# Kernel tuning notes

Hardware: AMD Instinct MI355X
Metric: run time of the kernel (lower is better)

## Reference

```python
import jax, jax.numpy as jnp
import numpy as np

N_NODES = 50000
N_EDGES = 800000
D_IN = 128
D_H = 128
N_LAYERS = 3
N_CLASSES = 10
NUM_GRAPHS = 256
BN_EPS = 1e-5


def _bn(h, gamma, beta):
    # BatchNorm1d, training-mode statistics (biased variance) over node axis
    mu = jnp.mean(h, axis=0)
    var = jnp.mean((h - mu) ** 2, axis=0)
    return (h - mu) * jax.lax.rsqrt(var + BN_EPS) * gamma + beta


def setup_inputs() -> dict:
    key = jax.random.key(0)
    ks = jax.random.split(key, 16)
    x = jax.random.normal(ks[0], (N_NODES, D_IN), dtype=jnp.float32)
    edge_index = jax.random.randint(ks[1], (2, N_EDGES), 0, N_NODES, dtype=jnp.int64)
    batch = jnp.sort(jax.random.randint(ks[2], (N_NODES,), 0, NUM_GRAPHS, dtype=jnp.int64))
    s1 = 1.0 / np.sqrt(D_IN)
    s2 = 1.0 / np.sqrt(D_H)
    W1 = jax.random.uniform(ks[3], (N_LAYERS, D_IN, D_H), jnp.float32, -s1, s1)
    b1 = jax.random.uniform(ks[4], (N_LAYERS, D_H), jnp.float32, -s1, s1)
    g1 = jnp.ones((N_LAYERS, D_H), jnp.float32)
    bt1 = jnp.zeros((N_LAYERS, D_H), jnp.float32)
    W2 = jax.random.uniform(ks[5], (N_LAYERS, D_H, D_H), jnp.float32, -s2, s2)
    b2 = jax.random.uniform(ks[6], (N_LAYERS, D_H), jnp.float32, -s2, s2)
    g2 = jnp.ones((N_LAYERS, D_H), jnp.float32)
    bt2 = jnp.zeros((N_LAYERS, D_H), jnp.float32)
    sc = 1.0 / np.sqrt(D_H * N_LAYERS)
    Wc1 = jax.random.uniform(ks[7], (D_H * N_LAYERS, D_H), jnp.float32, -sc, sc)
    bc1 = jax.random.uniform(ks[8], (D_H,), jnp.float32, -sc, sc)
    Wc2 = jax.random.uniform(ks[9], (D_H, N_CLASSES), jnp.float32, -s2, s2)
    bc2 = jax.random.uniform(ks[10], (N_CLASSES,), jnp.float32, -s2, s2)
    return {"x": x, "edge_index": edge_index, "batch": batch,
            "W1": W1, "b1": b1, "g1": g1, "bt1": bt1,
            "W2": W2, "b2": b2, "g2": g2, "bt2": bt2,
            "Wc1": Wc1, "bc1": bc1, "Wc2": Wc2, "bc2": bc2}


def reference(x, edge_index, batch, W1, b1, g1, bt1, W2, b2, g2, bt2, Wc1, bc1, Wc2, bc2):
    src = edge_index[0]
    dst = edge_index[1]
    readouts = []
    h = x
    for i in range(N_LAYERS):
        # GINConv, eps=0: (1+eps)*h + sum_{j->i} h_j, then MLP
        agg = jax.ops.segment_sum(h[src], dst, num_segments=N_NODES)  # [N, d]
        z = h + agg
        z = z @ W1[i] + b1[i]
        z = jax.nn.relu(_bn(z, g1[i], bt1[i]))
        z = z @ W2[i] + b2[i]
        # outer BN + ReLU
        h = jax.nn.relu(_bn(z, g2[i], bt2[i]))
        readouts.append(jax.ops.segment_sum(h, batch, num_segments=NUM_GRAPHS))
    h_graph = jnp.concatenate(readouts, axis=1)  # [G, L*d]
    # classifier (dropout in eval mode -> identity)
    out = jax.nn.relu(h_graph @ Wc1 + bc1) @ Wc2 + bc2
    return out
```

## Files before the change

### kernel.cpp

```cpp
#include <hip/hip_runtime.h>

#define N_NODES 50000
#define N_EDGES 800000
#define D 128
#define NLAYERS 3
#define N_CLASSES 10
#define NUM_GRAPHS 256
#define BN_EPS 1e-5f

#define CHUNKS 64
#define CHSIZE 12500
#define RANGES 4
#define RSIZE 12500
#define SBANKS 8

typedef __attribute__((ext_vector_type(4))) float f4;
typedef __attribute__((ext_vector_type(2))) float f2;
typedef __attribute__((ext_vector_type(8))) short short8;
typedef __attribute__((ext_vector_type(4))) unsigned short us4;
typedef __attribute__((ext_vector_type(8))) unsigned short us8;

__device__ inline float b2f(unsigned short u) {
    unsigned int i = ((unsigned int)u) << 16;
    return __builtin_bit_cast(float, i);
}
__device__ inline unsigned short f2b(float f) {
    unsigned int u = __builtin_bit_cast(unsigned int, f);
    unsigned int r = (u + 0x7FFFu + ((u >> 16) & 1u)) >> 16;
    return (unsigned short)r;
}

__device__ inline void coef_to_lds(const float* __restrict__ stats,
                                   const float* __restrict__ g,
                                   const float* __restrict__ bt,
                                   float* ac_sm, int tid) {
    if (tid < D) {
        float s = 0.f, q = 0.f;
#pragma unroll
        for (int b = 0; b < SBANKS; b++) {
            s += stats[b * 2 * D + tid];
            q += stats[b * 2 * D + D + tid];
        }
        float mu = s * (1.0f / N_NODES);
        float var = q * (1.0f / N_NODES) - mu * mu;
        float inv = rsqrtf(var + BN_EPS);
        float a = g[tid] * inv;
        ac_sm[tid] = a;
        ac_sm[D + tid] = bt[tid] - mu * a;
    }
}


__global__ __launch_bounds__(256) void k_ph(const int* __restrict__ dst,
                                            int* __restrict__ pos,
                                            int* __restrict__ ph) {
    __shared__ int h[RSIZE];
    int c = blockIdx.x, r = blockIdx.y;
    int t = threadIdx.x;
    for (int i = t; i < RSIZE; i += 256) h[i] = 0;
    __syncthreads();
    int base = c * CHSIZE;
    int lo = r * RSIZE;
    for (int j = t; j < CHSIZE; j += 256) {
        int d = dst[base + j] - lo;
        if ((unsigned)d < RSIZE) pos[base + j] = atomicAdd(&h[d], 1);
    }
    __syncthreads();
    int* outp = ph + (size_t)c * N_NODES + lo;
    for (int i = t; i < RSIZE; i += 256) outp[i] = h[i];
}

__global__ __launch_bounds__(256) void k_merge(int* __restrict__ ph, int* __restrict__ deg) {
    int b = blockIdx.x * 256 + threadIdx.x;
    if (b >= N_NODES) return;
    int s = 0;
#pragma unroll 4
    for (int c = 0; c < CHUNKS; c++) {
        int v = ph[(size_t)c * N_NODES + b];
        ph[(size_t)c * N_NODES + b] = s;
        s += v;
    }
    deg[b] = s;
}


__global__ __launch_bounds__(256) void k_xw(const float* __restrict__ x,
                                            const float* __restrict__ W1,
                                            const float* __restrict__ W2,
                                            us4* __restrict__ xb,
                                            short8* __restrict__ Wb) {
    int gid = blockIdx.x * 256 + threadIdx.x;
    const f4* xf = (const f4*)x;
#pragma unroll
    for (int rep = 0; rep < 2; rep++) {
        int i = gid + rep * 800000;
        f4 v = xf[i];
        us4 o;
        o[0] = f2b(v.x); o[1] = f2b(v.y); o[2] = f2b(v.z); o[3] = f2b(v.w);
        xb[i] = o;
    }
    if (gid < 6 * 32 * 64) {
        int m = gid >> 11;
        int f = (gid >> 6) & 31;
        int l = gid & 63;
        int ct = f >> 2, ks = f & 3;
        int n = ct * 16 + (l & 15);
        int k0 = ks * 32 + (l >> 4) * 8;
        const float* Wsrc = (m < 3) ? (W1 + (size_t)m * D * D) : (W2 + (size_t)(m - 3) * D * D);
        short8 o;
#pragma unroll
        for (int j = 0; j < 8; j++) o[j] = (short)f2b(Wsrc[(size_t)(k0 + j) * D + n]);
        Wb[gid] = o;
    }
}


__global__ void k_s1(const int* __restrict__ deg, const int* __restrict__ bat,
                     int* __restrict__ bsum, int* __restrict__ gp) {
    __shared__ int sm[256];
    int t = threadIdx.x;
    int i = blockIdx.x * 256 + t;
    int v = (i < N_NODES) ? deg[i] : 0;
    sm[t] = v;
    __syncthreads();
    for (int off = 128; off > 0; off >>= 1) {
        if (t < off) sm[t] += sm[t + off];
        __syncthreads();
    }
    if (t == 0) bsum[blockIdx.x] = sm[0];
    if (i < N_NODES) {
        int b = bat[i];
        int prev = (i == 0) ? -1 : bat[i - 1];
        for (int g = prev + 1; g <= b; g++) gp[g] = i;
        if (i == N_NODES - 1)
            for (int g = b + 1; g <= NUM_GRAPHS; g++) gp[g] = N_NODES;
    }
}

__global__ void k_s2(int* __restrict__ bsum, int* __restrict__ rowp) {
    __shared__ int sm[256];
    int t = threadIdx.x;
    int v = (t < 196) ? bsum[t] : 0;
    sm[t] = v;
    __syncthreads();
    for (int off = 1; off < 256; off <<= 1) {
        int u = (t >= off) ? sm[t - off] : 0;
        __syncthreads();
        sm[t] += u;
        __syncthreads();
    }
    if (t < 196) bsum[t] = sm[t] - v;
    if (t == 195) rowp[N_NODES] = sm[t];
}

__global__ void k_s3(const int* __restrict__ deg, const int* __restrict__ bsum,
                     int* __restrict__ rowp) {
    __shared__ int sm[256];
    int t = threadIdx.x;
    int i = blockIdx.x * 256 + t;
    int v = (i < N_NODES) ? deg[i] : 0;
    sm[t] = v;
    __syncthreads();
    for (int off = 1; off < 256; off <<= 1) {
        int u = (t >= off) ? sm[t - off] : 0;
        __syncthreads();
        sm[t] += u;
        __syncthreads();
    }
    if (i < N_NODES) rowp[i] = bsum[blockIdx.x] + sm[t] - v;
}

__global__ __launch_bounds__(256) void k_scatter(const int* __restrict__ src,
                                                 const int* __restrict__ dst,
                                                 const int* __restrict__ pos,
                                                 const int* __restrict__ ph,
                                                 const int* __restrict__ rowp,
                                                 int* __restrict__ csr) {
    int e = blockIdx.x * 256 + threadIdx.x;
    int c = e / CHSIZE;
    int d = dst[e];
    csr[rowp[d] + ph[(size_t)c * N_NODES + d] + pos[e]] = src[e];
}


template <bool APPLY_T>
__global__ __launch_bounds__(256) void k_agg(const us8* __restrict__ H,
                                             const float* __restrict__ stats,
                                             const float* __restrict__ g,
                                             const float* __restrict__ bt,
                                             const int* __restrict__ rowp,
                                             const int* __restrict__ csr,
                                             us8* __restrict__ U) {
    __shared__ float ac_sm[2 * D];
    int tid = threadIdx.x;
    if (APPLY_T) {
        coef_to_lds(stats, g, bt, ac_sm, tid);
        __syncthreads();
    }
    int gid = blockIdx.x * 256 + tid;
    int node = gid >> 4;
    int lane = tid & 15;
    float av[8], cv[8];
    if (APPLY_T) {
#pragma unroll
        for (int i = 0; i < 8; i++) {
            av[i] = ac_sm[lane * 8 + i];
            cv[i] = ac_sm[D + lane * 8 + i];
        }
    }
    float s[8] = {0.f, 0.f, 0.f, 0.f, 0.f, 0.f, 0.f, 0.f};
    auto accum = [&](us8 v) {
#pragma unroll
        for (int i = 0; i < 8; i++) {
            float f = b2f(v[i]);
            if (APPLY_T) f = fmaxf(f * av[i] + cv[i], 0.f);
            s[i] += f;
        }
    };
    accum(H[(size_t)node * 16 + lane]);
    int beg = rowp[node], end = rowp[node + 1];
    int j = beg;
    for (; j + 4 <= end; j += 4) {
        int i0 = csr[j], i1 = csr[j + 1], i2 = csr[j + 2], i3 = csr[j + 3];
        us8 v0 = H[(size_t)i0 * 16 + lane];
        us8 v1 = H[(size_t)i1 * 16 + lane];
        us8 v2 = H[(size_t)i2 * 16 + lane];
        us8 v3 = H[(size_t)i3 * 16 + lane];
        accum(v0); accum(v1); accum(v2); accum(v3);
    }
    for (; j < end; j++) accum(H[(size_t)csr[j] * 16 + lane]);
    us8 o;
#pragma unroll
    for (int i = 0; i < 8; i++) o[i] = f2b(s[i]);
    U[(size_t)node * 16 + lane] = o;
}


template <bool TRANS>
__global__ __launch_bounds__(256) void k_gemm(const unsigned short* __restrict__ A,
                                              const short8* __restrict__ Wb,
                                              const float* __restrict__ bias,
                                              const float* __restrict__ stats_in,
                                              const float* __restrict__ g,
                                              const float* __restrict__ bt,
                                              unsigned short* __restrict__ Z,
                                              float* __restrict__ stats_out, int M) {
    __shared__ float lds_s[D], lds_q[D];
    __shared__ float ac_sm[2 * D];
    int tid = threadIdx.x;
    if (tid < D) { lds_s[tid] = 0.f; lds_q[tid] = 0.f; }
    if (TRANS) coef_to_lds(stats_in, g, bt, ac_sm, tid);
    int w = tid >> 6, l = tid & 63;
    int lr = l & 15, lg = l >> 4;
    int rowb0 = blockIdx.x * 128 + w * 32;
    f4 acc[2][8];
#pragma unroll
    for (int ct = 0; ct < 8; ct++) {
        float bv = bias[ct * 16 + lr];
#pragma unroll
        for (int rt = 0; rt < 2; rt++) {
            acc[rt][ct].x = bv; acc[rt][ct].y = bv; acc[rt][ct].z = bv; acc[rt][ct].w = bv;
        }
    }
    __syncthreads();

#pragma unroll
    for (int ks = 0; ks < 4; ks++) {
        short8 a[2];
#pragma unroll
        for (int rt = 0; rt < 2; rt++) {
            int arow = rowb0 + rt * 16 + lr;
            int arow_c = arow < M ? arow : M - 1;
            if (!TRANS) {
                a[rt] = *(const short8*)(A + (size_t)arow_c * D + ks * 32 + lg * 8);
            } else {
                int k0 = ks * 32 + lg * 8;
                const unsigned short* ap = A + (size_t)arow_c * D + k0;
                us4 v0 = *(const us4*)ap;
                us4 v1 = *(const us4*)(ap + 4);
                f4 a0 = *(const f4*)&ac_sm[k0];
                f4 a1 = *(const f4*)&ac_sm[k0 + 4];
                f4 c0 = *(const f4*)&ac_sm[D + k0];
                f4 c1 = *(const f4*)&ac_sm[D + k0 + 4];
                a[rt][0] = (short)f2b(fmaxf(b2f(v0[0]) * a0.x + c0.x, 0.f));
                a[rt][1] = (short)f2b(fmaxf(b2f(v0[1]) * a0.y + c0.y, 0.f));
                a[rt][2] = (short)f2b(fmaxf(b2f(v0[2]) * a0.z + c0.z, 0.f));
                a[rt][3] = (short)f2b(fmaxf(b2f(v0[3]) * a0.w + c0.w, 0.f));
                a[rt][4] = (short)f2b(fmaxf(b2f(v1[0]) * a1.x + c1.x, 0.f));
                a[rt][5] = (short)f2b(fmaxf(b2f(v1[1]) * a1.y + c1.y, 0.f));
                a[rt][6] = (short)f2b(fmaxf(b2f(v1[2]) * a1.z + c1.z, 0.f));
                a[rt][7] = (short)f2b(fmaxf(b2f(v1[3]) * a1.w + c1.w, 0.f));
            }
        }
#pragma unroll
        for (int ct = 0; ct < 8; ct++) {
            short8 b = Wb[(ct * 4 + ks) * 64 + l];
            acc[0][ct] = __builtin_amdgcn_mfma_f32_16x16x32_bf16(a[0], b, acc[0][ct], 0, 0, 0);
            acc[1][ct] = __builtin_amdgcn_mfma_f32_16x16x32_bf16(a[1], b, acc[1][ct], 0, 0, 0);
        }
    }

#pragma unroll
    for (int ct = 0; ct < 8; ct++) {
        float s = 0.f, q = 0.f;
#pragma unroll
        for (int rt = 0; rt < 2; rt++) {
#pragma unroll
            for (int r = 0; r < 4; r++) {
                float v = acc[rt][ct][r];
                int rd = rowb0 + rt * 16 + lg * 4 + r;
                float m = rd < M ? 1.f : 0.f;
                s += v * m;
                q += v * v * m;
                if (rd < M) Z[(size_t)rd * D + ct * 16 + lr] = f2b(v);
            }
        }
        s += __shfl_xor(s, 16);
        s += __shfl_xor(s, 32);
        q += __shfl_xor(q, 16);
        q += __shfl_xor(q, 32);
        if (lg == 0) {
            atomicAdd(&lds_s[ct * 16 + lr], s);
            atomicAdd(&lds_q[ct * 16 + lr], q);
        }
    }
    __syncthreads();
    int bank = blockIdx.x & (SBANKS - 1);
    if (tid < D) {
        atomicAdd(&stats_out[bank * 2 * D + tid], lds_s[tid]);
        atomicAdd(&stats_out[bank * 2 * D + D + tid], lds_q[tid]);
    }
}


__global__ __launch_bounds__(256) void k_readout(const unsigned int* __restrict__ Zb,
                                                 const float* __restrict__ stats,
                                                 const float* __restrict__ g,
                                                 const float* __restrict__ bt,
                                                 const int* __restrict__ gp,
                                                 const int* __restrict__ batch,
                                                 float* __restrict__ ro, int layer) {
    __shared__ f2 sm[256];
    __shared__ float ac_sm[2 * D];
    int tid = threadIdx.x;
    coef_to_lds(stats, g, bt, ac_sm, tid);
    __syncthreads();
    int n0 = blockIdx.x * 256;
    int n1 = n0 + 256; if (n1 > N_NODES) n1 = N_NODES;
    int g_lo = batch[n0], g_hi = batch[n1 - 1];
    int grp = tid >> 6, cw = tid & 63;
    float a0 = ac_sm[2 * cw], a1 = ac_sm[2 * cw + 1];
    float c0 = ac_sm[D + 2 * cw], c1 = ac_sm[D + 2 * cw + 1];
    for (int gg = g_lo; gg <= g_hi; gg++) {
        int beg = gp[gg]; if (beg < n0) beg = n0;
        int end = gp[gg + 1]; if (end > n1) end = n1;
        f2 acc; acc.x = 0.f; acc.y = 0.f;
        for (int r = beg + grp; r < end; r += 4) {
            unsigned int v = Zb[(size_t)r * 64 + cw];
            float x0 = b2f((unsigned short)(v & 0xFFFFu));
            float x1 = b2f((unsigned short)(v >> 16));
            acc.x += fmaxf(x0 * a0 + c0, 0.f);
            acc.y += fmaxf(x1 * a1 + c1, 0.f);
        }
        sm[tid] = acc;
        __syncthreads();
        if (tid < 64) {
            f2 t = sm[tid];
            t.x += sm[tid + 64].x + sm[tid + 128].x + sm[tid + 192].x;
            t.y += sm[tid + 64].y + sm[tid + 128].y + sm[tid + 192].y;
            atomicAdd(&ro[(size_t)gg * (NLAYERS * D) + layer * D + 2 * cw], t.x);
            atomicAdd(&ro[(size_t)gg * (NLAYERS * D) + layer * D + 2 * cw + 1], t.y);
        }
        __syncthreads();
    }
}


__global__ void k_cls(const float* __restrict__ ro, const float* __restrict__ Wc1,
                      const float* __restrict__ bc1, const float* __restrict__ Wc2,
                      const float* __restrict__ bc2, float* __restrict__ out) {
    __shared__ float r_sm[NLAYERS * D];
    __shared__ float h_sm[D];
    int g = blockIdx.x;
    int t = threadIdx.x;
    for (int i = t; i < NLAYERS * D; i += D) r_sm[i] = ro[(size_t)g * (NLAYERS * D) + i];
    __syncthreads();
    float acc = bc1[t];
    for (int k = 0; k < NLAYERS * D; k++) acc += r_sm[k] * Wc1[(size_t)k * D + t];
    h_sm[t] = fmaxf(acc, 0.f);
    __syncthreads();
    if (t < N_CLASSES) {
        float o = bc2[t];
        for (int k = 0; k < D; k++) o += h_sm[k] * Wc2[k * N_CLASSES + t];
        out[g * N_CLASSES + t] = o;
    }
}


extern "C" void kernel_launch(void* const* d_in, const int* in_sizes, int n_in,
                              void* d_out, int out_size, void* d_ws, size_t ws_size,
                              hipStream_t stream) {
    const float* x   = (const float*)d_in[0];
    const int*   ei  = (const int*)d_in[1];
    const int*   bat = (const int*)d_in[2];
    const float* W1  = (const float*)d_in[3];
    const float* b1  = (const float*)d_in[4];
    const float* g1  = (const float*)d_in[5];
    const float* bt1 = (const float*)d_in[6];
    const float* W2  = (const float*)d_in[7];
    const float* b2  = (const float*)d_in[8];
    const float* g2  = (const float*)d_in[9];
    const float* bt2 = (const float*)d_in[10];
    const float* Wc1 = (const float*)d_in[11];
    const float* bc1 = (const float*)d_in[12];
    const float* Wc2 = (const float*)d_in[13];
    const float* bc2 = (const float*)d_in[14];
    float* out = (float*)d_out;

    const int* src = ei;
    const int* dst = ei + N_EDGES;

    char* ws = (char*)d_ws;
    size_t off = 0;
    auto alloc = [&](size_t bytes) -> void* {
        void* p = ws + off;
        off += (bytes + 255) & ~(size_t)255;
        return p;
    };
    float* stats = (float*)alloc(6 * SBANKS * 2 * D * sizeof(float));
    float* ro    = (float*)alloc((size_t)NUM_GRAPHS * NLAYERS * D * sizeof(float));
    size_t zero_bytes = off;
    int*   deg   = (int*)alloc(N_NODES * sizeof(int));
    int*   gp    = (int*)alloc((NUM_GRAPHS + 1) * sizeof(int));
    int*   bsum  = (int*)alloc(256 * sizeof(int));
    int*   rowp  = (int*)alloc((N_NODES + 1) * sizeof(int));
    int*   pos   = (int*)alloc(N_EDGES * sizeof(int));
    int*   csr   = (int*)alloc(N_EDGES * sizeof(int));
    const size_t NBH = (size_t)N_NODES * D * sizeof(unsigned short);
    unsigned short* xb   = (unsigned short*)alloc(NBH);
    unsigned short* bufA = (unsigned short*)alloc(NBH);
    unsigned short* bufB = (unsigned short*)alloc(NBH);
    unsigned short* bufC = (unsigned short*)alloc(NBH);
    short8* Wb   = (short8*)alloc(6 * 32 * 64 * sizeof(short8));
    int* ph = (int*)bufB;

    hipMemsetAsync(ws, 0, zero_bytes, stream);

    k_ph<<<dim3(CHUNKS, RANGES), 256, 0, stream>>>(dst, pos, ph);
    k_merge<<<196, 256, 0, stream>>>(ph, deg);
    k_xw<<<3125, 256, 0, stream>>>(x, W1, W2, (us4*)xb, Wb);
    k_s1<<<196, 256, 0, stream>>>(deg, bat, bsum, gp);
    k_s2<<<1, 256, 0, stream>>>(bsum, rowp);
    k_s3<<<196, 256, 0, stream>>>(deg, bsum, rowp);
    k_scatter<<<3125, 256, 0, stream>>>(src, dst, pos, ph, rowp, csr);

    const int gemm_grid = (N_NODES + 127) / 128;
    const unsigned short* H = xb;
    for (int i = 0; i < NLAYERS; i++) {
        float* st1 = stats + (size_t)(2 * i) * SBANKS * 2 * D;
        float* st2 = stats + (size_t)(2 * i + 1) * SBANKS * 2 * D;
        float* st2p = stats + (size_t)(2 * i - 1) * SBANKS * 2 * D;
        if (i == 0)
            k_agg<false><<<3125, 256, 0, stream>>>((const us8*)H, nullptr, nullptr, nullptr,
                                                   rowp, csr, (us8*)bufA);
        else
            k_agg<true><<<3125, 256, 0, stream>>>((const us8*)H, st2p, g2 + (i - 1) * D,
                                                  bt2 + (i - 1) * D, rowp, csr, (us8*)bufA);
        k_gemm<false><<<gemm_grid, 256, 0, stream>>>(bufA, Wb + (size_t)i * 2048, b1 + i * D,
                                                     nullptr, nullptr, nullptr, bufB, st1, N_NODES);
        k_gemm<true><<<gemm_grid, 256, 0, stream>>>(bufB, Wb + (size_t)(3 + i) * 2048, b2 + i * D,
                                                    st1, g1 + i * D, bt1 + i * D, bufC, st2, N_NODES);
        k_readout<<<196, 256, 0, stream>>>((const unsigned int*)bufC, st2, g2 + i * D, bt2 + i * D,
                                           gp, bat, ro, i);
        H = bufC;
    }
    k_cls<<<NUM_GRAPHS, 128, 0, stream>>>(ro, Wc1, bc1, Wc2, bc2, out);
}
```

Measured before the change: 343.1 us.

## Fuse merge with block-sum scan, vectorize CSR build, deepen aggregation gather unroll

Merges the per-chunk prefix merge kernel with the degree block-sum and graph-pointer kernel, removing one launch and a re-read of the degree array. The histogram and scatter kernels now load dst/src/pos as 4-wide int vectors, with each thread handling four edges. The aggregation gather loop is unrolled to 8 neighbors with all indices and rows loaded before accumulation, which gives more memory parallelism per thread at the cost of extra registers. These target the preprocessing overhead and the latency-bound neighbor gather.

```diff
diff --git a/kernel.cpp b/kernel.cpp
--- a/kernel.cpp
+++ b/kernel.cpp
@@ -16,6 +16,7 @@
 
 typedef __attribute__((ext_vector_type(4))) float f4;
 typedef __attribute__((ext_vector_type(2))) float f2;
+typedef __attribute__((ext_vector_type(4))) int i4;
 typedef __attribute__((ext_vector_type(8))) short short8;
 typedef __attribute__((ext_vector_type(4))) unsigned short us4;
 typedef __attribute__((ext_vector_type(8))) unsigned short us8;
@@ -61,26 +62,52 @@
     __syncthreads();
     int base = c * CHSIZE;
     int lo = r * RSIZE;
-    for (int j = t; j < CHSIZE; j += 256) {
-        int d = dst[base + j] - lo;
-        if ((unsigned)d < RSIZE) pos[base + j] = atomicAdd(&h[d], 1);
+    const i4* dst4 = (const i4*)(dst + base);
+    for (int j = t; j < CHSIZE / 4; j += 256) {
+        i4 dv = dst4[j];
+#pragma unroll
+        for (int u = 0; u < 4; u++) {
+            int d = dv[u] - lo;
+            if ((unsigned)d < RSIZE) pos[base + j * 4 + u] = atomicAdd(&h[d], 1);
+        }
     }
     __syncthreads();
     int* outp = ph + (size_t)c * N_NODES + lo;
     for (int i = t; i < RSIZE; i += 256) outp[i] = h[i];
 }
 
-__global__ __launch_bounds__(256) void k_merge(int* __restrict__ ph, int* __restrict__ deg) {
-    int b = blockIdx.x * 256 + threadIdx.x;
-    if (b >= N_NODES) return;
+__global__ __launch_bounds__(256) void k_m1(int* __restrict__ ph,
+                                            const int* __restrict__ bat,
+                                            int* __restrict__ deg,
+                                            int* __restrict__ bsum,
+                                            int* __restrict__ gp) {
+    __shared__ int sm[256];
+    int t = threadIdx.x;
+    int b = blockIdx.x * 256 + t;
     int s = 0;
+    if (b < N_NODES) {
 #pragma unroll 4
-    for (int c = 0; c < CHUNKS; c++) {
-        int v = ph[(size_t)c * N_NODES + b];
-        ph[(size_t)c * N_NODES + b] = s;
-        s += v;
-    }
-    deg[b] = s;
+        for (int c = 0; c < CHUNKS; c++) {
+            int v = ph[(size_t)c * N_NODES + b];
+            ph[(size_t)c * N_NODES + b] = s;
+            s += v;
+        }
+        deg[b] = s;
+    }
+    sm[t] = s;
+    __syncthreads();
+    for (int off = 128; off > 0; off >>= 1) {
+        if (t < off) sm[t] += sm[t + off];
+        __syncthreads();
+    }
+    if (t == 0) bsum[blockIdx.x] = sm[0];
+    if (b < N_NODES) {
+        int bb = bat[b];
+        int prev = (b == 0) ? -1 : bat[b - 1];
+        for (int g = prev + 1; g <= bb; g++) gp[g] = b;
+        if (b == N_NODES - 1)
+            for (int g = bb + 1; g <= NUM_GRAPHS; g++) gp[g] = N_NODES;
+    }
 }
 
 
@@ -115,28 +142,6 @@
 }
 
 
-__global__ void k_s1(const int* __restrict__ deg, const int* __restrict__ bat,
-                     int* __restrict__ bsum, int* __restrict__ gp) {
-    __shared__ int sm[256];
-    int t = threadIdx.x;
-    int i = blockIdx.x * 256 + t;
-    int v = (i < N_NODES) ? deg[i] : 0;
-    sm[t] = v;
-    __syncthreads();
-    for (int off = 128; off > 0; off >>= 1) {
-        if (t < off) sm[t] += sm[t + off];
-        __syncthreads();
-    }
-    if (t == 0) bsum[blockIdx.x] = sm[0];
-    if (i < N_NODES) {
-        int b = bat[i];
-        int prev = (i == 0) ? -1 : bat[i - 1];
-        for (int g = prev + 1; g <= b; g++) gp[g] = i;
-        if (i == N_NODES - 1)
-            for (int g = b + 1; g <= NUM_GRAPHS; g++) gp[g] = N_NODES;
-    }
-}
-
 __global__ void k_s2(int* __restrict__ bsum, int* __restrict__ rowp) {
     __shared__ int sm[256];
     int t = threadIdx.x;
@@ -176,10 +181,17 @@
                                                  const int* __restrict__ ph,
                                                  const int* __restrict__ rowp,
                                                  int* __restrict__ csr) {
-    int e = blockIdx.x * 256 + threadIdx.x;
-    int c = e / CHSIZE;
-    int d = dst[e];
-    csr[rowp[d] + ph[(size_t)c * N_NODES + d] + pos[e]] = src[e];
+    int e0 = (blockIdx.x * 256 + threadIdx.x) * 4;
+    if (e0 >= N_EDGES) return;
+    i4 sv = *(const i4*)(src + e0);
+    i4 dv = *(const i4*)(dst + e0);
+    i4 pv = *(const i4*)(pos + e0);
+#pragma unroll
+    for (int u = 0; u < 4; u++) {
+        int cc = (e0 + u) / CHSIZE;
+        int d = dv[u];
+        csr[rowp[d] + ph[(size_t)cc * N_NODES + d] + pv[u]] = sv[u];
+    }
 }
 
 
@@ -220,15 +232,23 @@
     accum(H[(size_t)node * 16 + lane]);
     int beg = rowp[node], end = rowp[node + 1];
     int j = beg;
-    for (; j + 4 <= end; j += 4) {
-        int i0 = csr[j], i1 = csr[j + 1], i2 = csr[j + 2], i3 = csr[j + 3];
+    for (; j + 8 <= end; j += 8) {
+        int idx[8];
+#pragma unroll
+        for (int u = 0; u < 8; u++) idx[u] = csr[j + u];
+        us8 v[8];
+#pragma unroll
+        for (int u = 0; u < 8; u++) v[u] = H[(size_t)idx[u] * 16 + lane];
+#pragma unroll
+        for (int u = 0; u < 8; u++) accum(v[u]);
+    }
+    for (; j + 2 <= end; j += 2) {
+        int i0 = csr[j], i1 = csr[j + 1];
         us8 v0 = H[(size_t)i0 * 16 + lane];
         us8 v1 = H[(size_t)i1 * 16 + lane];
-        us8 v2 = H[(size_t)i2 * 16 + lane];
-        us8 v3 = H[(size_t)i3 * 16 + lane];
-        accum(v0); accum(v1); accum(v2); accum(v3);
-    }
-    for (; j < end; j++) accum(H[(size_t)csr[j] * 16 + lane]);
+        accum(v0); accum(v1);
+    }
+    if (j < end) accum(H[(size_t)csr[j] * 16 + lane]);
     us8 o;
 #pragma unroll
     for (int i = 0; i < 8; i++) o[i] = f2b(s[i]);
@@ -447,12 +467,11 @@
     hipMemsetAsync(ws, 0, zero_bytes, stream);
 
     k_ph<<<dim3(CHUNKS, RANGES), 256, 0, stream>>>(dst, pos, ph);
-    k_merge<<<196, 256, 0, stream>>>(ph, deg);
+    k_m1<<<196, 256, 0, stream>>>(ph, bat, deg, bsum, gp);
     k_xw<<<3125, 256, 0, stream>>>(x, W1, W2, (us4*)xb, Wb);
-    k_s1<<<196, 256, 0, stream>>>(deg, bat, bsum, gp);
     k_s2<<<1, 256, 0, stream>>>(bsum, rowp);
     k_s3<<<196, 256, 0, stream>>>(deg, bsum, rowp);
-    k_scatter<<<3125, 256, 0, stream>>>(src, dst, pos, ph, rowp, csr);
+    k_scatter<<<(N_EDGES / 4 + 255) / 256, 256, 0, stream>>>(src, dst, pos, ph, rowp, csr);
 
     const int gemm_grid = (N_NODES + 127) / 128;
     const unsigned short* H = xb;
```

New measurement: 346.7 us. No clear change (+1.0%).
